# Kernel tuning notes

Hardware: AMD Instinct MI355X
Metric: run time of the kernel (lower is better)

## Reference

```python
import jax, jax.numpy as jnp
import numpy as np

BETA = 0.25  # commitment cost
EPS = 1e-10


def _vq_layer(xf, cb):
    # xf: [M, D] flattened features, cb: [K, D] codebook
    K = cb.shape[0]
    M = xf.shape[0]
    d = (jnp.sum(xf * xf, axis=-1, keepdims=True)
         - 2.0 * (xf @ cb.T)
         + jnp.sum(cb * cb, axis=-1))
    idx = jnp.argmin(d, axis=-1)          # [M]
    q = cb[idx]                           # [M, D]
    # commitment + codebook loss (VQ-VAE)
    commit = jnp.mean((jax.lax.stop_gradient(q) - xf) ** 2)
    cbloss = jnp.mean((q - jax.lax.stop_gradient(xf)) ** 2)
    loss = cbloss + BETA * commit
    # straight-through estimator
    q_st = xf + jax.lax.stop_gradient(q - xf)
    # codebook usage perplexity
    counts = jnp.zeros((K,), dtype=xf.dtype).at[idx].add(1.0)
    p = counts / M
    perplexity = jnp.exp(-jnp.sum(p * jnp.log(p + EPS)))
    return q_st, idx, loss, perplexity


def setup_inputs() -> dict:
    key = jax.random.key(0)
    k1, k2 = jax.random.split(key)
    B, N, D, H, W, K = 32, 4, 128, 32, 32, 1024
    x = jax.random.normal(k1, (B, N * D, H, W), dtype=jnp.float32)
    codebooks = jax.random.normal(k2, (N, K, D), dtype=jnp.float32)
    return {"x": x, "codebooks": codebooks}


def reference(x, codebooks):
    B, C, H, W = x.shape
    N, K, D = codebooks.shape
    assert C == N * D
    M = B * H * W
    # [B, N*D, H, W] -> [N, M, D]
    xs = x.reshape(B, N, D, H, W).transpose(1, 0, 3, 4, 2).reshape(N, M, D)
    q, idx, loss, perp = jax.vmap(_vq_layer)(xs, codebooks)
    # quantized_cat: [N, M, D] -> [B, N*D, H, W]  (cat along channel dim)
    quantized_cat = (q.reshape(N, B, H, W, D)
                      .transpose(1, 0, 4, 2, 3)
                      .reshape(B, N * D, H, W))
    # indices_cat: [N, M] -> [B, N, H, W]
    indices_cat = idx.reshape(N, B, H, W).transpose(1, 0, 2, 3)
    return quantized_cat, indices_cat, loss, perp
```

## Files before the change

kernel.cpp:

```cpp
#include <hip/hip_runtime.h>

#define B_ 32
#define N_ 4
#define D_ 128
#define M_ 32768
#define K_ 1024

#define IDX_OFF 16777216
#define LOSS_OFF 16908288
#define PERP_OFF 16908292

#define WS_LOSS 0
#define WS_CNT 1024
#define WS_ENORM 8192
#define WS_BPACK_F 16384
#define BPACK_LAYER_US 262144

#define SBIAS 384.0f
#define MARGIN 0.012f

typedef __bf16 bf16x8 __attribute__((ext_vector_type(8)));
typedef float f32x4 __attribute__((ext_vector_type(4)));

union FragU {
  bf16x8 v;
  ushort u16[8];
  uint4 q;
};

__device__ __forceinline__ ushort bf16_hi_rne(float f, float* hif) {
  uint u = __float_as_uint(f);
  uint r = (u + 0x7fffu + ((u >> 16) & 1u)) >> 16;
  *hif = __uint_as_float(r << 16);
  return (ushort)r;
}
__device__ __forceinline__ ushort bf16_rne(float f) {
  uint u = __float_as_uint(f);
  return (ushort)((u + 0x7fffu + ((u >> 16) & 1u)) >> 16);
}

__device__ __forceinline__ void gload_lds16(const void* g, void* l) {
  __builtin_amdgcn_global_load_lds(
      (const __attribute__((address_space(1))) unsigned int*)g,
      (__attribute__((address_space(3))) unsigned int*)l, 16, 0, 0);
}

__global__ void vq_pack(const float* __restrict__ cb, float* __restrict__ ws) {
  int blk = blockIdx.x, tid = threadIdx.x;
  if (blk < 256) {
    int n = blk >> 6, tile = blk & 63;
    int s = tid >> 6, lane = tid & 63;
    int code = tile * 16 + (lane & 15);
    int dbase = s * 32 + ((lane >> 4) << 3);
    const float* src = cb + ((size_t)(n * K_ + code)) * D_ + dbase;
    float4 v0 = *(const float4*)src;
    float4 v1 = *(const float4*)(src + 4);
    float v[8] = {v0.x, v0.y, v0.z, v0.w, v1.x, v1.y, v1.z, v1.w};
    FragU fh, fl;
#pragma unroll
    for (int j = 0; j < 8; ++j) {
      float hif;
      fh.u16[j] = bf16_hi_rne(v[j], &hif);
      fl.u16[j] = bf16_rne(v[j] - hif);
    }
    ushort* base = (ushort*)(ws + WS_BPACK_F) + (size_t)n * BPACK_LAYER_US +
                   ((size_t)(tile * 4 + s) * 2) * 512 + lane * 8;
    *(uint4*)base = fh.q;
    *(uint4*)(base + 512) = fl.q;
  } else if (blk < 1280) {
    int lane = tid & 63, w = tid >> 6;
    int waveid = (blk - 256) * 4 + w;
    int n = waveid >> 10, k = waveid & 1023;
    const float2* row = (const float2*)(cb + (size_t)(n * K_ + k) * D_);
    float2 v = row[lane];
    float ss = fmaf(v.x, v.x, v.y * v.y);
#pragma unroll
    for (int off = 32; off; off >>= 1) ss += __shfl_down(ss, off, 64);
    if (lane == 0) ws[WS_ENORM + n * K_ + k] = SBIAS - 0.5f * ss;
  } else {
#pragma unroll
    for (int i = 0; i < 20; ++i) ws[i * 256 + tid] = 0.f;
  }
}

__global__ __launch_bounds__(256, 4) void vq_main(const float* __restrict__ x,
                                                  const float* __restrict__ cb,
                                                  float* __restrict__ ws,
                                                  float* __restrict__ out) {
  __shared__ alignas(16) ushort Bsm[18432];
  const int tid = threadIdx.x;
  const int bid = blockIdx.x;
  const int n = bid >> 8;
  const int mblk = bid & 255;
  const int b = mblk >> 3;
  const int hw0 = (mblk & 7) << 7;

  const int lane = tid & 63, w = tid >> 6;
  const int quad = lane >> 4, l15 = lane & 15;

  const float* xbase = x + (size_t)((b * 4 + n) * 128) * 1024 + hw0;
  const float* cbn = cb + (size_t)n * K_ * D_;
  const float* enB = ws + WS_ENORM + n * K_;
  const ushort* bpack_n = (ushort*)(ws + WS_BPACK_F) + (size_t)n * BPACK_LAYER_US;

  char* ext = (char*)Bsm + 32768;
  int* sIdx = (int*)ext;
  float* dist = (float*)(ext + 512);
  int* list = (int*)(ext + 1024);
  int* lcnt = (int*)(ext + 1536);
  double* xrowd = (double*)(ext + 1544);
  double* rd = (double*)(ext + 2568);
  int* rk = (int*)(ext + 2600);

  if (tid == 0) *lcnt = 0;

  bf16x8 ahi[2][4], alo[2][4];
#pragma unroll
  for (int set = 0; set < 2; ++set) {
    const int hwl = w * 32 + set * 16 + l15;
    float xs = 0.f;
#pragma unroll
    for (int s = 0; s < 4; ++s) {
      const int dbase = s * 32 + quad * 8;
      FragU fh, fl;
#pragma unroll
      for (int j = 0; j < 8; ++j) {
        float v = xbase[(size_t)(dbase + j) * 1024 + hwl];
        xs = fmaf(v, v, xs);
        float hif;
        fh.u16[j] = bf16_hi_rne(v, &hif);
        fl.u16[j] = bf16_rne(v - hif);
      }
      ahi[set][s] = fh.v;
      alo[set][s] = fl.v;
    }
    xs += __shfl_xor(xs, 16, 64);
    xs += __shfl_xor(xs, 32, 64);
    if (l15 == lane) dist[w * 32 + set * 16 + l15] = xs;
  }

  uint best[8], best2[8];
#pragma unroll
  for (int i = 0; i < 8; ++i) { best[i] = 0u; best2[i] = 0u; }

  const uint4* gsrc = (const uint4*)bpack_n;
  uint4* Bsm4 = (uint4*)Bsm;

#pragma unroll
  for (int i = 0; i < 4; ++i)
    gload_lds16(gsrc + i * 256 + w * 64 + lane, Bsm4 + i * 256 + w * 64);

#pragma unroll 1
  for (int c = 0; c < 32; ++c) {
    __syncthreads();
    if (c < 31) {
      const uint4* src = gsrc + (c + 1) * 1024;
      uint4* dst = Bsm4 + ((c + 1) & 1) * 1024;
#pragma unroll
      for (int i = 0; i < 4; ++i)
        gload_lds16(src + i * 256 + w * 64 + lane, dst + i * 256 + w * 64);
    }
    const ushort* Bcur = Bsm + (c & 1) * 8192;
#pragma unroll
    for (int tin = 0; tin < 2; ++tin) {
      const int t = c * 2 + tin;
      const uint tinv = (uint)(63 - t);
      float en = enB[t * 16 + l15];
      bf16x8 bh[4], bl[4];
#pragma unroll
      for (int s = 0; s < 4; ++s) {
        const ushort* p = Bcur + ((tin * 4 + s) * 2) * 512 + lane * 8;
        bh[s] = ((const FragU*)p)->v;
        bl[s] = ((const FragU*)(p + 512))->v;
      }
      f32x4 acc[2];
#pragma unroll
      for (int set = 0; set < 2; ++set) acc[set] = (f32x4){0.f, 0.f, 0.f, 0.f};
#pragma unroll
      for (int s = 0; s < 4; ++s) {
#pragma unroll
        for (int set = 0; set < 2; ++set)
          acc[set] = __builtin_amdgcn_mfma_f32_16x16x32_bf16(ahi[set][s], bh[s], acc[set], 0, 0, 0);
#pragma unroll
        for (int set = 0; set < 2; ++set)
          acc[set] = __builtin_amdgcn_mfma_f32_16x16x32_bf16(ahi[set][s], bl[s], acc[set], 0, 0, 0);
#pragma unroll
        for (int set = 0; set < 2; ++set)
          acc[set] = __builtin_amdgcn_mfma_f32_16x16x32_bf16(alo[set][s], bh[s], acc[set], 0, 0, 0);
      }
#pragma unroll
      for (int set = 0; set < 2; ++set) {
#pragma unroll
        for (int r = 0; r < 4; ++r) {
          float sb = acc[set][r] + en;
          uint key = (__float_as_uint(sb) & 0xFFFFFFC0u) | tinv;
          uint ob = best[set * 4 + r];
          uint mn = key < ob ? key : ob;
          best[set * 4 + r] = key > ob ? key : ob;
          if (mn > best2[set * 4 + r]) best2[set * 4 + r] = mn;
        }
      }
    }
  }
  __syncthreads();

  uint* sS = (uint*)Bsm;
  uint* sS2 = (uint*)((char*)Bsm + 8704);
#pragma unroll
  for (int set = 0; set < 2; ++set) {
#pragma unroll
    for (int r = 0; r < 4; ++r) {
      int m = w * 32 + set * 16 + quad * 4 + r;
      sS[m * 17 + l15] = best[set * 4 + r];
      sS2[m * 17 + l15] = best2[set * 4 + r];
    }
  }
  __syncthreads();

  if (tid < 128) {
    int m = tid;
    uint g1 = 0, g2 = 0;
    int gi = 0;
#pragma unroll 4
    for (int li = 0; li < 16; ++li) {
      uint key = sS[m * 17 + li];
      uint sb = key >> 6;
      int kk = (int)(63u - (key & 63u)) * 16 + li;
      if (sb > g1) { g2 = g1; g1 = sb; gi = kk; }
      else {
        if (sb == g1 && kk < gi) gi = kk;
        if (sb > g2) g2 = sb;
      }
      uint sb2 = sS2[m * 17 + li] >> 6;
      if (sb2 > g2) g2 = sb2;
    }
    sIdx[m] = gi;
    float s1f = __uint_as_float(g1 << 6);
    dist[m] = dist[m] - 2.0f * (s1f - SBIAS);
    float gap = s1f - __uint_as_float(g2 << 6);
    if (gap < MARGIN) {
      int pos = atomicAdd(lcnt, 1);
      list[pos] = m;
    }
  }
  __syncthreads();

  const int cnt = *lcnt;
  for (int i = 0; i < cnt; ++i) {
    const int m = list[i];
    if (tid < 128) xrowd[tid] = (double)xbase[(size_t)tid * 1024 + m];
    __syncthreads();
    double bd = 1e300;
    int bk = 0;
#pragma unroll 1
    for (int j = 0; j < 4; ++j) {
      const int k = tid * 4 + j;
      const float4* er = (const float4*)(cbn + (size_t)k * D_);
      double d = 0.0;
#pragma unroll 8
      for (int c4 = 0; c4 < 32; ++c4) {
        float4 e = er[c4];
        double d0 = xrowd[c4 * 4 + 0] - (double)e.x;
        double d1 = xrowd[c4 * 4 + 1] - (double)e.y;
        double d2 = xrowd[c4 * 4 + 2] - (double)e.z;
        double d3 = xrowd[c4 * 4 + 3] - (double)e.w;
        d = fma(d0, d0, d);
        d = fma(d1, d1, d);
        d = fma(d2, d2, d);
        d = fma(d3, d3, d);
      }
      if (d < bd) { bd = d; bk = k; }
    }
#pragma unroll
    for (int off = 32; off; off >>= 1) {
      double od = __shfl_down(bd, off, 64);
      int ok = __shfl_down(bk, off, 64);
      if (od < bd || (od == bd && ok < bk)) { bd = od; bk = ok; }
    }
    if (lane == 0) { rd[w] = bd; rk[w] = bk; }
    __syncthreads();
    if (tid == 0) {
      double gb = rd[0];
      int gk = rk[0];
      for (int t = 1; t < 4; ++t)
        if (rd[t] < gb || (rd[t] == gb && rk[t] < gk)) { gb = rd[t]; gk = rk[t]; }
      sIdx[m] = gk;
      dist[m] = (float)gb;
    }
    __syncthreads();
  }

  if (tid < 128) {
    int bi = sIdx[tid];
    out[IDX_OFF + (b * 4 + n) * 1024 + hw0 + tid] = (float)bi;
    atomicAdd(ws + WS_CNT + n * K_ + bi, 1.0f);
  }
  float lp = (tid < 128) ? dist[tid] : 0.f;
#pragma unroll
  for (int off = 32; off; off >>= 1) lp += __shfl_down(lp, off, 64);
  if (lane == 0 && w < 2) atomicAdd(ws + WS_LOSS + n, lp);
  __syncthreads();

  float* Qs = (float*)Bsm;
  float* out0 = out + (size_t)((b * 4 + n) * 128) * 1024 + hw0;
#pragma unroll 1
  for (int h = 0; h < 2; ++h) {
    const int m = tid & 127, part = tid >> 7;
    const float* src = cbn + (size_t)sIdx[m] * D_ + h * 64 + part * 32;
#pragma unroll
    for (int i = 0; i < 8; ++i) {
      float4 v = ((const float4*)src)[i];
      int dl = part * 32 + i * 4;
      Qs[(dl + 0) * 128 + m] = v.x;
      Qs[(dl + 1) * 128 + m] = v.y;
      Qs[(dl + 2) * 128 + m] = v.z;
      Qs[(dl + 3) * 128 + m] = v.w;
    }
    __syncthreads();
#pragma unroll
    for (int it = 0; it < 8; ++it) {
      int e = it * 256 + tid;
      int m4 = (e & 31) * 4;
      int dl = e >> 5;
      float4 v = *(float4*)(Qs + dl * 128 + m4);
      *(float4*)(out0 + (size_t)(h * 64 + dl) * 1024 + m4) = v;
    }
    __syncthreads();
  }
}

__global__ void vq_finalize(const float* __restrict__ ws, float* __restrict__ out) {
  int n = blockIdx.x;
  int t = threadIdx.x;
  const float* counts = ws + WS_CNT + n * K_;
  float s = 0.f;
  for (int k = t; k < K_; k += 256) {
    float p = counts[k] * (1.0f / 32768.0f);
    s += p * logf(p + 1e-10f);
  }
  __shared__ float red[4];
#pragma unroll
  for (int off = 32; off; off >>= 1) s += __shfl_down(s, off, 64);
  if ((t & 63) == 0) red[t >> 6] = s;
  __syncthreads();
  if (t == 0) {
    s = red[0] + red[1] + red[2] + red[3];
    out[PERP_OFF + n] = expf(-s);
    out[LOSS_OFF + n] = 1.25f * ws[WS_LOSS + n] / 4194304.0f;
  }
}

extern "C" void kernel_launch(void* const* d_in, const int* in_sizes, int n_in,
                              void* d_out, int out_size, void* d_ws, size_t ws_size,
                              hipStream_t stream) {
  const float* x = (const float*)d_in[0];
  const float* cb = (const float*)d_in[1];
  float* out = (float*)d_out;
  float* ws = (float*)d_ws;
  vq_pack<<<1281, 256, 0, stream>>>(cb, ws);
  vq_main<<<1024, 256, 0, stream>>>(x, cb, ws, out);
  vq_finalize<<<4, 256, 0, stream>>>(ws, out);
}
```

Baseline: 276.5 us.

## Read packed codebook directly from global/L2, drop LDS staging, remap blocks per XCD

The main kernel stops staging packed bf16 codebook tiles into LDS with async global-to-LDS loads and barriers. Each wave now reads its B fragments straight from global memory, relying on L2 since every block of a layer reuses the same packed codebook. Block IDs are remapped so each XCD handles a single layer, which keeps that layer's codebook resident in its L2. LDS use drops to about 20KB (the quantized-output transpose now runs in four quarters), which may allow more resident blocks. The pack kernel now also computes codebook norms through shared memory, cutting its grid from 1281 to 257 blocks; the cost is more global load traffic and latency inside the MFMA loop.

```diff
diff --git a/kernel.cpp b/kernel.cpp
--- a/kernel.cpp
+++ b/kernel.cpp
@@ -39,44 +39,47 @@
   return (ushort)((u + 0x7fffu + ((u >> 16) & 1u)) >> 16);
 }
 
-__device__ __forceinline__ void gload_lds16(const void* g, void* l) {
-  __builtin_amdgcn_global_load_lds(
-      (const __attribute__((address_space(1))) unsigned int*)g,
-      (__attribute__((address_space(3))) unsigned int*)l, 16, 0, 0);
-}
-
-__global__ void vq_pack(const float* __restrict__ cb, float* __restrict__ ws) {
+__global__ __launch_bounds__(256) void vq_pack(const float* __restrict__ cb,
+                                               float* __restrict__ ws) {
+  __shared__ ushort Hs[16 * 132];
+  __shared__ ushort Ls[16 * 132];
+  __shared__ float Ps[256];
   int blk = blockIdx.x, tid = threadIdx.x;
   if (blk < 256) {
     int n = blk >> 6, tile = blk & 63;
-    int s = tid >> 6, lane = tid & 63;
-    int code = tile * 16 + (lane & 15);
-    int dbase = s * 32 + ((lane >> 4) << 3);
-    const float* src = cb + ((size_t)(n * K_ + code)) * D_ + dbase;
+    int c = tid >> 4, f = tid & 15;
+    const float* src = cb + ((size_t)(n * K_ + tile * 16 + c)) * D_ + f * 8;
     float4 v0 = *(const float4*)src;
     float4 v1 = *(const float4*)(src + 4);
     float v[8] = {v0.x, v0.y, v0.z, v0.w, v1.x, v1.y, v1.z, v1.w};
-    FragU fh, fl;
+    float ss = 0.f;
 #pragma unroll
     for (int j = 0; j < 8; ++j) {
       float hif;
-      fh.u16[j] = bf16_hi_rne(v[j], &hif);
-      fl.u16[j] = bf16_rne(v[j] - hif);
-    }
-    ushort* base = (ushort*)(ws + WS_BPACK_F) + (size_t)n * BPACK_LAYER_US +
-                   ((size_t)(tile * 4 + s) * 2) * 512 + lane * 8;
-    *(uint4*)base = fh.q;
-    *(uint4*)(base + 512) = fl.q;
-  } else if (blk < 1280) {
-    int lane = tid & 63, w = tid >> 6;
-    int waveid = (blk - 256) * 4 + w;
-    int n = waveid >> 10, k = waveid & 1023;
-    const float2* row = (const float2*)(cb + (size_t)(n * K_ + k) * D_);
-    float2 v = row[lane];
-    float ss = fmaf(v.x, v.x, v.y * v.y);
-#pragma unroll
-    for (int off = 32; off; off >>= 1) ss += __shfl_down(ss, off, 64);
-    if (lane == 0) ws[WS_ENORM + n * K_ + k] = SBIAS - 0.5f * ss;
+      Hs[c * 132 + f * 8 + j] = bf16_hi_rne(v[j], &hif);
+      Ls[c * 132 + f * 8 + j] = bf16_rne(v[j] - hif);
+      ss = fmaf(v[j], v[j], ss);
+    }
+    Ps[c * 16 + f] = ss;
+    __syncthreads();
+    if (tid < 16) {
+      float s = 0.f;
+#pragma unroll
+      for (int j = 0; j < 16; ++j) s += Ps[tid * 16 + j];
+      ws[WS_ENORM + n * K_ + tile * 16 + tid] = SBIAS - 0.5f * s;
+    }
+    int s = tid >> 6, lane = tid & 63;
+    int code = lane & 15, dstart = s * 32 + ((lane >> 4) << 3);
+    FragU fh, fl;
+#pragma unroll
+    for (int j = 0; j < 8; ++j) {
+      fh.u16[j] = Hs[code * 132 + dstart + j];
+      fl.u16[j] = Ls[code * 132 + dstart + j];
+    }
+    ushort* dst = (ushort*)(ws + WS_BPACK_F) + (size_t)n * BPACK_LAYER_US +
+                  ((size_t)(tile * 4 + s) * 2) * 512 + lane * 8;
+    *(uint4*)dst = fh.q;
+    *(uint4*)(dst + 512) = fl.q;
   } else {
 #pragma unroll
     for (int i = 0; i < 20; ++i) ws[i * 256 + tid] = 0.f;
@@ -87,11 +90,12 @@
                                                   const float* __restrict__ cb,
                                                   float* __restrict__ ws,
                                                   float* __restrict__ out) {
-  __shared__ alignas(16) ushort Bsm[18432];
+  __shared__ alignas(16) uint Lds[5120];
   const int tid = threadIdx.x;
   const int bid = blockIdx.x;
-  const int n = bid >> 8;
-  const int mblk = bid & 255;
+  const int xcd = bid & 7;
+  const int n = xcd >> 1;
+  const int mblk = (xcd & 1) * 128 + (bid >> 3);
   const int b = mblk >> 3;
   const int hw0 = (mblk & 7) << 7;
 
@@ -101,16 +105,18 @@
   const float* xbase = x + (size_t)((b * 4 + n) * 128) * 1024 + hw0;
   const float* cbn = cb + (size_t)n * K_ * D_;
   const float* enB = ws + WS_ENORM + n * K_;
-  const ushort* bpack_n = (ushort*)(ws + WS_BPACK_F) + (size_t)n * BPACK_LAYER_US;
-
-  char* ext = (char*)Bsm + 32768;
-  int* sIdx = (int*)ext;
-  float* dist = (float*)(ext + 512);
-  int* list = (int*)(ext + 1024);
-  int* lcnt = (int*)(ext + 1536);
-  double* xrowd = (double*)(ext + 1544);
-  double* rd = (double*)(ext + 2568);
-  int* rk = (int*)(ext + 2600);
+  const uint4* gB = (const uint4*)((ushort*)(ws + WS_BPACK_F) + (size_t)n * BPACK_LAYER_US);
+
+  uint* sS = Lds;
+  uint* sS2 = Lds + 2176;
+  int* sIdx = (int*)(Lds + 4352);
+  float* dist = (float*)(Lds + 4480);
+  int* list = (int*)(Lds + 4608);
+  int* lcnt = (int*)(Lds + 4736);
+  double* xrowd = (double*)(Lds + 4740);
+  double* rd = (double*)(Lds + 4996);
+  int* rk = (int*)(Lds + 5004);
+  float* Qs = (float*)Lds;
 
   if (tid == 0) *lcnt = 0;
 
@@ -136,76 +142,57 @@
     }
     xs += __shfl_xor(xs, 16, 64);
     xs += __shfl_xor(xs, 32, 64);
-    if (l15 == lane) dist[w * 32 + set * 16 + l15] = xs;
+    if (lane < 16) dist[w * 32 + set * 16 + l15] = xs;
   }
 
   uint best[8], best2[8];
 #pragma unroll
   for (int i = 0; i < 8; ++i) { best[i] = 0u; best2[i] = 0u; }
 
-  const uint4* gsrc = (const uint4*)bpack_n;
-  uint4* Bsm4 = (uint4*)Bsm;
-
-#pragma unroll
-  for (int i = 0; i < 4; ++i)
-    gload_lds16(gsrc + i * 256 + w * 64 + lane, Bsm4 + i * 256 + w * 64);
-
 #pragma unroll 1
-  for (int c = 0; c < 32; ++c) {
-    __syncthreads();
-    if (c < 31) {
-      const uint4* src = gsrc + (c + 1) * 1024;
-      uint4* dst = Bsm4 + ((c + 1) & 1) * 1024;
-#pragma unroll
-      for (int i = 0; i < 4; ++i)
-        gload_lds16(src + i * 256 + w * 64 + lane, dst + i * 256 + w * 64);
-    }
-    const ushort* Bcur = Bsm + (c & 1) * 8192;
-#pragma unroll
-    for (int tin = 0; tin < 2; ++tin) {
-      const int t = c * 2 + tin;
-      const uint tinv = (uint)(63 - t);
-      float en = enB[t * 16 + l15];
-      bf16x8 bh[4], bl[4];
-#pragma unroll
-      for (int s = 0; s < 4; ++s) {
-        const ushort* p = Bcur + ((tin * 4 + s) * 2) * 512 + lane * 8;
-        bh[s] = ((const FragU*)p)->v;
-        bl[s] = ((const FragU*)(p + 512))->v;
+  for (int t = 0; t < 64; ++t) {
+    const uint tinv = (uint)(63 - t);
+    float en = enB[t * 16 + l15];
+    const uint4* pb = gB + t * 512 + lane;
+    bf16x8 bh[4], bl[4];
+#pragma unroll
+    for (int s = 0; s < 4; ++s) {
+      FragU fh, fl;
+      fh.q = pb[s * 128];
+      fl.q = pb[s * 128 + 64];
+      bh[s] = fh.v;
+      bl[s] = fl.v;
+    }
+    f32x4 acc[2];
+#pragma unroll
+    for (int set = 0; set < 2; ++set) acc[set] = (f32x4){0.f, 0.f, 0.f, 0.f};
+#pragma unroll
+    for (int s = 0; s < 4; ++s) {
+#pragma unroll
+      for (int set = 0; set < 2; ++set)
+        acc[set] = __builtin_amdgcn_mfma_f32_16x16x32_bf16(ahi[set][s], bh[s], acc[set], 0, 0, 0);
+#pragma unroll
+      for (int set = 0; set < 2; ++set)
+        acc[set] = __builtin_amdgcn_mfma_f32_16x16x32_bf16(ahi[set][s], bl[s], acc[set], 0, 0, 0);
+#pragma unroll
+      for (int set = 0; set < 2; ++set)
+        acc[set] = __builtin_amdgcn_mfma_f32_16x16x32_bf16(alo[set][s], bh[s], acc[set], 0, 0, 0);
+    }
+#pragma unroll
+    for (int set = 0; set < 2; ++set) {
+#pragma unroll
+      for (int r = 0; r < 4; ++r) {
+        float sb = acc[set][r] + en;
+        uint key = (__float_as_uint(sb) & 0xFFFFFFC0u) | tinv;
+        uint ob = best[set * 4 + r];
+        uint mn = key < ob ? key : ob;
+        best[set * 4 + r] = key > ob ? key : ob;
+        if (mn > best2[set * 4 + r]) best2[set * 4 + r] = mn;
       }
-      f32x4 acc[2];
-#pragma unroll
-      for (int set = 0; set < 2; ++set) acc[set] = (f32x4){0.f, 0.f, 0.f, 0.f};
-#pragma unroll
-      for (int s = 0; s < 4; ++s) {
-#pragma unroll
-        for (int set = 0; set < 2; ++set)
-          acc[set] = __builtin_amdgcn_mfma_f32_16x16x32_bf16(ahi[set][s], bh[s], acc[set], 0, 0, 0);
-#pragma unroll
-        for (int set = 0; set < 2; ++set)
-          acc[set] = __builtin_amdgcn_mfma_f32_16x16x32_bf16(ahi[set][s], bl[s], acc[set], 0, 0, 0);
-#pragma unroll
-        for (int set = 0; set < 2; ++set)
-          acc[set] = __builtin_amdgcn_mfma_f32_16x16x32_bf16(alo[set][s], bh[s], acc[set], 0, 0, 0);
-      }
-#pragma unroll
-      for (int set = 0; set < 2; ++set) {
-#pragma unroll
-        for (int r = 0; r < 4; ++r) {
-          float sb = acc[set][r] + en;
-          uint key = (__float_as_uint(sb) & 0xFFFFFFC0u) | tinv;
-          uint ob = best[set * 4 + r];
-          uint mn = key < ob ? key : ob;
-          best[set * 4 + r] = key > ob ? key : ob;
-          if (mn > best2[set * 4 + r]) best2[set * 4 + r] = mn;
-        }
-      }
-    }
-  }
-  __syncthreads();
-
-  uint* sS = (uint*)Bsm;
-  uint* sS2 = (uint*)((char*)Bsm + 8704);
+    }
+  }
+
+  __syncthreads();
 #pragma unroll
   for (int set = 0; set < 2; ++set) {
 #pragma unroll
@@ -301,16 +288,15 @@
   if (lane == 0 && w < 2) atomicAdd(ws + WS_LOSS + n, lp);
   __syncthreads();
 
-  float* Qs = (float*)Bsm;
   float* out0 = out + (size_t)((b * 4 + n) * 128) * 1024 + hw0;
 #pragma unroll 1
-  for (int h = 0; h < 2; ++h) {
+  for (int q = 0; q < 4; ++q) {
     const int m = tid & 127, part = tid >> 7;
-    const float* src = cbn + (size_t)sIdx[m] * D_ + h * 64 + part * 32;
-#pragma unroll
-    for (int i = 0; i < 8; ++i) {
+    const float* src = cbn + (size_t)sIdx[m] * D_ + q * 32 + part * 16;
+#pragma unroll
+    for (int i = 0; i < 4; ++i) {
       float4 v = ((const float4*)src)[i];
-      int dl = part * 32 + i * 4;
+      int dl = part * 16 + i * 4;
       Qs[(dl + 0) * 128 + m] = v.x;
       Qs[(dl + 1) * 128 + m] = v.y;
       Qs[(dl + 2) * 128 + m] = v.z;
@@ -318,12 +304,12 @@
     }
     __syncthreads();
 #pragma unroll
-    for (int it = 0; it < 8; ++it) {
+    for (int it = 0; it < 4; ++it) {
       int e = it * 256 + tid;
       int m4 = (e & 31) * 4;
       int dl = e >> 5;
       float4 v = *(float4*)(Qs + dl * 128 + m4);
-      *(float4*)(out0 + (size_t)(h * 64 + dl) * 1024 + m4) = v;
+      *(float4*)(out0 + (size_t)(q * 32 + dl) * 1024 + m4) = v;
     }
     __syncthreads();
   }
@@ -357,7 +343,7 @@
   const float* cb = (const float*)d_in[1];
   float* out = (float*)d_out;
   float* ws = (float*)d_ws;
-  vq_pack<<<1281, 256, 0, stream>>>(cb, ws);
+  vq_pack<<<257, 256, 0, stream>>>(cb, ws);
   vq_main<<<1024, 256, 0, stream>>>(x, cb, ws, out);
   vq_finalize<<<4, 256, 0, stream>>>(ws, out);
 }
```

Result: slower. 310.0 us (+12.1%).
